# Optimization experiments

Hardware: AMD Instinct MI355X
Metric: run time of the kernel (lower is better)

Reference implementation:

```python
import jax, jax.numpy as jnp
import numpy as np

EMBED = 1024
HEADS = 16
HEAD_DIM = EMBED // HEADS
FF = 4 * EMBED
B, S = 2, 2048


def setup_inputs() -> dict:
    key = jax.random.key(0)
    ks = jax.random.split(key, 16)
    sd = 0.02
    inp = {
        "x": jax.random.normal(ks[0], (B, S, EMBED), dtype=jnp.float32),
        "Wq": jax.random.normal(ks[1], (EMBED, EMBED), dtype=jnp.float32) * sd,
        "bq": jnp.zeros((EMBED,), jnp.float32),
        "Wk": jax.random.normal(ks[2], (EMBED, EMBED), dtype=jnp.float32) * sd,
        "bk": jnp.zeros((EMBED,), jnp.float32),
        "Wv": jax.random.normal(ks[3], (EMBED, EMBED), dtype=jnp.float32) * sd,
        "bv": jnp.zeros((EMBED,), jnp.float32),
        "Wo": jax.random.normal(ks[4], (EMBED, EMBED), dtype=jnp.float32) * sd,
        "W1": jax.random.normal(ks[5], (EMBED, FF), dtype=jnp.float32) * sd,
        "b1": jnp.zeros((FF,), jnp.float32),
        "W2": jax.random.normal(ks[6], (FF, EMBED), dtype=jnp.float32) * sd,
        "b2": jnp.zeros((EMBED,), jnp.float32),
        "g1": jnp.ones((EMBED,), jnp.float32),
        "be1": jnp.zeros((EMBED,), jnp.float32),
        "g2": jnp.ones((EMBED,), jnp.float32),
        "be2": jnp.zeros((EMBED,), jnp.float32),
    }
    return inp


def _layernorm(x, g, b, eps=1e-5):
    mu = jnp.mean(x, axis=-1, keepdims=True)
    var = jnp.mean(jnp.square(x - mu), axis=-1, keepdims=True)
    return (x - mu) * jax.lax.rsqrt(var + eps) * g + b


def _attn(x, Wq, bq, Wk, bk, Wv, bv, Wo):
    b, s, d = x.shape
    q = (x @ Wq + bq).reshape(b, s, HEADS, HEAD_DIM)
    k = (x @ Wk + bk).reshape(b, s, HEADS, HEAD_DIM)
    v = (x @ Wv + bv).reshape(b, s, HEADS, HEAD_DIM)
    # NOTE: original scales by sqrt(embed_dim), NOT sqrt(head_dim)
    logits = jnp.einsum('bqhd,bkhd->bhqk', q, k) / jnp.sqrt(jnp.float32(d))
    mask = jnp.tril(jnp.ones((s, s), dtype=bool))
    logits = jnp.where(mask, logits, -jnp.inf)
    w = jax.nn.softmax(logits, axis=-1)
    z = jnp.einsum('bhqk,bkhd->bqhd', w, v).reshape(b, s, d)
    return z @ Wo


def reference(x, Wq, bq, Wk, bk, Wv, bv, Wo, W1, b1, W2, b2, g1, be1, g2, be2):
    h = x + _attn(_layernorm(x, g1, be1), Wq, bq, Wk, bk, Wv, bv, Wo)
    m = _layernorm(h, g2, be2)
    m = jax.nn.gelu(m @ W1 + b1, approximate=False) @ W2 + b2
    return h + m
```

## Files before the change

kernel.cpp:

```cpp
#include <hip/hip_runtime.h>
#include <cstdint>
#include <cstddef>
#include <math.h>

#define EMBED 1024
#define SEQ   2048
#define NROWS 4096
#define NHEADS 16

typedef __bf16 bf16x8 __attribute__((ext_vector_type(8)));
typedef float f32x4 __attribute__((ext_vector_type(4)));
typedef unsigned short us8 __attribute__((ext_vector_type(8)));
typedef unsigned short us4 __attribute__((ext_vector_type(4)));

__device__ __forceinline__ unsigned short f2bf(float f) {
  union { float f; unsigned u; } v; v.f = f;
  unsigned r = v.u + 0x7fffu + ((v.u >> 16) & 1u);
  return (unsigned short)(r >> 16);
}

__device__ __forceinline__ bf16x8 as_bf(us8 u) { return __builtin_bit_cast(bf16x8, u); }

__device__ __forceinline__ void gload_lds16(const unsigned short* g, unsigned short* l) {
  __builtin_amdgcn_global_load_lds((const __attribute__((address_space(1))) void*)g,
                                   (__attribute__((address_space(3))) void*)l, 16, 0, 0);
}

__global__ __launch_bounds__(256) void transpose_to_bf16(
    const float* __restrict__ in, unsigned short* __restrict__ out, int K, int N) {
  __shared__ float tile[32][33];
  const int tx = threadIdx.x & 31, ty = threadIdx.x >> 5;
  const int n0 = blockIdx.x * 32, k0 = blockIdx.y * 32;
#pragma unroll
  for (int i = 0; i < 4; i++) {
    int k = ty + i * 8;
    tile[k][tx] = in[(size_t)(k0 + k) * N + n0 + tx];
  }
  __syncthreads();
#pragma unroll
  for (int i = 0; i < 4; i++) {
    int n = ty + i * 8;
    out[(size_t)(n0 + n) * K + k0 + tx] = f2bf(tile[tx][n]);
  }
}

__global__ __launch_bounds__(256) void layernorm_bf16(
    const float* __restrict__ x, const float* __restrict__ g,
    const float* __restrict__ be, unsigned short* __restrict__ out) {
  const int wave = threadIdx.x >> 6, lane = threadIdx.x & 63;
  const int row = blockIdx.x * 4 + wave;
  const float* xr = x + (size_t)row * EMBED;
  float4 v[4];
  float s = 0.f, sq = 0.f;
#pragma unroll
  for (int c = 0; c < 4; c++) {
    v[c] = *(const float4*)&xr[c * 256 + lane * 4];
    s  += v[c].x + v[c].y + v[c].z + v[c].w;
    sq += v[c].x * v[c].x + v[c].y * v[c].y + v[c].z * v[c].z + v[c].w * v[c].w;
  }
#pragma unroll
  for (int m = 1; m < 64; m <<= 1) {
    s  += __shfl_xor(s, m, 64);
    sq += __shfl_xor(sq, m, 64);
  }
  const float mean = s * (1.f / 1024.f);
  const float var  = sq * (1.f / 1024.f) - mean * mean;
  const float rstd = rsqrtf(var + 1e-5f);
#pragma unroll
  for (int c = 0; c < 4; c++) {
    const int idx = c * 256 + lane * 4;
    us4 o;
    o[0] = f2bf((v[c].x - mean) * rstd * g[idx + 0] + be[idx + 0]);
    o[1] = f2bf((v[c].y - mean) * rstd * g[idx + 1] + be[idx + 1]);
    o[2] = f2bf((v[c].z - mean) * rstd * g[idx + 2] + be[idx + 2]);
    o[3] = f2bf((v[c].w - mean) * rstd * g[idx + 3] + be[idx + 3]);
    *(us4*)&out[(size_t)row * EMBED + idx] = o;
  }
}

enum { MODE_QKV = 0, MODE_WO = 1, MODE_FF1 = 2, MODE_FF2 = 3 };

template <int MODE>
__global__ __launch_bounds__(256) void gemm_bf16(
    const unsigned short* __restrict__ A,
    const unsigned short* __restrict__ Bt0,
    const unsigned short* __restrict__ Bt1,
    const unsigned short* __restrict__ Bt2,
    const float* __restrict__ bias0,
    const float* __restrict__ bias1,
    const float* __restrict__ bias2,
    const float* __restrict__ res,
    void* __restrict__ out0, void* __restrict__ out1, void* __restrict__ out2,
    int M, int N, int K) {
  const unsigned short* Bt = Bt0;
  const float* bias = bias0;
  void* outv = out0;
  int zidx = 0;
  if constexpr (MODE == MODE_QKV) {
    zidx = blockIdx.z;
    if (zidx == 1)      { Bt = Bt1; bias = bias1; outv = out1; }
    else if (zidx == 2) { Bt = Bt2; bias = bias2; outv = out2; }
  }
  __shared__ unsigned short As[128 * 32];
  __shared__ unsigned short Bs[128 * 32];
  const int tid = threadIdx.x;
  const int wave = tid >> 6, lane = tid & 63;
  const int quad = lane >> 4, l15 = lane & 15;
  const int wr = (wave >> 1) * 64, wc = (wave & 1) * 64;
  const int rowA0 = blockIdx.y * 128, colB0 = blockIdx.x * 128;

  const int srow = tid >> 2;
  const int scol = (tid & 3) * 8;
  const unsigned short* gA = A  + (size_t)(rowA0 + srow) * K + scol;
  const unsigned short* gB = Bt + (size_t)(colB0 + srow) * K + scol;
  unsigned short* lA  = &As[tid * 8];
  unsigned short* lA2 = &As[2048 + tid * 8];
  unsigned short* lB  = &Bs[tid * 8];
  unsigned short* lB2 = &Bs[2048 + tid * 8];
  const size_t half = (size_t)64 * K;

  f32x4 acc[4][4];
#pragma unroll
  for (int i = 0; i < 4; i++)
#pragma unroll
    for (int j = 0; j < 4; j++) acc[i][j] = f32x4{0.f, 0.f, 0.f, 0.f};

  for (int k0 = 0; k0 < K; k0 += 32) {
    gload_lds16(gA + k0, lA);
    gload_lds16(gA + half + k0, lA2);
    gload_lds16(gB + k0, lB);
    gload_lds16(gB + half + k0, lB2);
    __syncthreads();
    bf16x8 af[4], bfr[4];
#pragma unroll
    for (int mi = 0; mi < 4; mi++)
      af[mi] = as_bf(*(const us8*)&As[(wr + mi * 16 + l15) * 32 + quad * 8]);
#pragma unroll
    for (int ni = 0; ni < 4; ni++)
      bfr[ni] = as_bf(*(const us8*)&Bs[(wc + ni * 16 + l15) * 32 + quad * 8]);
#pragma unroll
    for (int mi = 0; mi < 4; mi++)
#pragma unroll
      for (int ni = 0; ni < 4; ni++)
        acc[mi][ni] = __builtin_amdgcn_mfma_f32_16x16x32_bf16(af[mi], bfr[ni], acc[mi][ni], 0, 0, 0);
    __syncthreads();
  }

#pragma unroll
  for (int ni = 0; ni < 4; ni++) {
    const int col = colB0 + wc + ni * 16 + l15;
    float bv = 0.f;
    if constexpr (MODE != MODE_WO) bv = bias[col];
#pragma unroll
    for (int mi = 0; mi < 4; mi++) {
      const int row0 = rowA0 + wr + mi * 16 + quad * 4;
      if constexpr (MODE == MODE_QKV) {
        unsigned short* o = (unsigned short*)outv;
        if (zidx == 2) {
          us4 pk;
#pragma unroll
          for (int r = 0; r < 4; r++) pk[r] = f2bf(acc[mi][ni][r] + bv);
          const int bb = row0 >> 11;
          const int sr = row0 & 2047;
          *(us4*)&o[((size_t)(bb * 1024 + col)) * SEQ + sr] = pk;
        } else {
#pragma unroll
          for (int r = 0; r < 4; r++)
            o[(size_t)(row0 + r) * N + col] = f2bf(acc[mi][ni][r] + bv);
        }
      } else if constexpr (MODE == MODE_FF1) {
        unsigned short* o = (unsigned short*)outv;
#pragma unroll
        for (int r = 0; r < 4; r++) {
          float v = acc[mi][ni][r] + bv;
          v = 0.5f * v * (1.f + erff(v * 0.7071067811865476f));
          o[(size_t)(row0 + r) * N + col] = f2bf(v);
        }
      } else {
        float* o = (float*)outv;
#pragma unroll
        for (int r = 0; r < 4; r++) {
          float v = acc[mi][ni][r] + bv + res[(size_t)(row0 + r) * N + col];
          o[(size_t)(row0 + r) * N + col] = v;
        }
      }
    }
  }
}

__global__ __launch_bounds__(256) void attn_kernel(
    const unsigned short* __restrict__ Q,
    const unsigned short* __restrict__ Kb,
    const unsigned short* __restrict__ Vt,
    unsigned short* __restrict__ Z) {
  __shared__ unsigned short Ksh[2][64][32];
  __shared__ unsigned short Vsh[2][64][32];
  __shared__ unsigned short Pt[4][16][72];
  __shared__ float Ot[4][64][17];

  const int wave = threadIdx.x >> 6, lane = threadIdx.x & 63;
  const int quad = lane >> 4, l15 = lane & 15;
  const int bh = blockIdx.x, b = bh >> 4, h = bh & 15;
  const int qt = blockIdx.y;
  const int q0 = qt * 128 + wave * 32;
  const float cscale = 1.4426950408889634f / 32.f;

  bf16x8 qf[2][2];
#pragma unroll
  for (int c = 0; c < 2; c++)
#pragma unroll
    for (int kf = 0; kf < 2; kf++)
      qf[c][kf] = as_bf(*(const us8*)&Q[(size_t)(b * SEQ + q0 + c * 16 + l15) * EMBED +
                                        h * 64 + kf * 32 + quad * 8]);

  f32x4 accO[2][4];
#pragma unroll
  for (int c = 0; c < 2; c++)
#pragma unroll
    for (int dt = 0; dt < 4; dt++) accO[c][dt] = f32x4{0.f, 0.f, 0.f, 0.f};
  float mrun[2] = {-INFINITY, -INFINITY};
  float lrun[2] = {0.f, 0.f};

  const int ls_row = lane >> 2;
  const int ls_c16 = lane & 3;
  const int nkt = 2 * qt + 2;

  for (int kt = 0; kt < nkt; kt++) {
    const int kbase = kt * 64;
    const int krow = wave * 16 + ls_row;
#pragma unroll
    for (int kf = 0; kf < 2; kf++) {
      const unsigned short* g =
          &Kb[(size_t)(b * SEQ + kbase + krow) * EMBED + h * 64 + kf * 32 + ls_c16 * 8];
      gload_lds16(g, &Ksh[kf][wave * 16][0] + lane * 8);
    }
#pragma unroll
    for (int kk = 0; kk < 2; kk++) {
      const unsigned short* g =
          &Vt[(size_t)(b * 1024 + h * 64 + krow) * SEQ + kbase + kk * 32 + ls_c16 * 8];
      gload_lds16(g, &Vsh[kk][wave * 16][0] + lane * 8);
    }
    __syncthreads();

#pragma unroll
    for (int c = 0; c < 2; c++) {
      const int qc = q0 + c * 16;
      if (kbase > qc + 15) continue;
      f32x4 sf[4];
#pragma unroll
      for (int nt = 0; nt < 4; nt++) {
        f32x4 z4 = f32x4{0.f, 0.f, 0.f, 0.f};
#pragma unroll
        for (int kf = 0; kf < 2; kf++) {
          const bf16x8 ka = as_bf(*(const us8*)&Ksh[kf][nt * 16 + l15][quad * 8]);
          z4 = __builtin_amdgcn_mfma_f32_16x16x32_bf16(ka, qf[c][kf], z4, 0, 0, 0);
        }
        sf[nt] = z4 * cscale;
      }
      if (kbase + 63 > qc) {
        const int q = qc + l15;
#pragma unroll
        for (int nt = 0; nt < 4; nt++) {
          const int key0 = kbase + nt * 16 + quad * 4;
#pragma unroll
          for (int r = 0; r < 4; r++)
            if (key0 + r > q) sf[nt][r] = -INFINITY;
        }
      }
      float mx = sf[0][0];
#pragma unroll
      for (int nt = 0; nt < 4; nt++)
#pragma unroll
        for (int r = 0; r < 4; r++) mx = fmaxf(mx, sf[nt][r]);
      mx = fmaxf(mx, __shfl_xor(mx, 16, 64));
      mx = fmaxf(mx, __shfl_xor(mx, 32, 64));
      const float mnew = fmaxf(mrun[c], mx);
      const float alpha = exp2f(mrun[c] - mnew);
      mrun[c] = mnew;
      float rs = 0.f;
#pragma unroll
      for (int nt = 0; nt < 4; nt++) {
        us4 pk;
#pragma unroll
        for (int r = 0; r < 4; r++) {
          const float p = exp2f(sf[nt][r] - mnew);
          rs += p;
          pk[r] = f2bf(p);
        }
        *(us4*)&Pt[wave][l15][nt * 16 + quad * 4] = pk;
      }
      rs += __shfl_xor(rs, 16, 64);
      rs += __shfl_xor(rs, 32, 64);
      lrun[c] = lrun[c] * alpha + rs;
#pragma unroll
      for (int dt = 0; dt < 4; dt++) accO[c][dt] = accO[c][dt] * alpha;
      bf16x8 pf[2];
#pragma unroll
      for (int kk = 0; kk < 2; kk++)
        pf[kk] = as_bf(*(const us8*)&Pt[wave][l15][kk * 32 + quad * 8]);
#pragma unroll
      for (int dt = 0; dt < 4; dt++)
#pragma unroll
        for (int kk = 0; kk < 2; kk++) {
          const bf16x8 va = as_bf(*(const us8*)&Vsh[kk][dt * 16 + l15][quad * 8]);
          accO[c][dt] = __builtin_amdgcn_mfma_f32_16x16x32_bf16(va, pf[kk], accO[c][dt], 0, 0, 0);
        }
    }
    __syncthreads();
  }

#pragma unroll
  for (int c = 0; c < 2; c++) {
    const float inv = 1.f / lrun[c];
#pragma unroll
    for (int dt = 0; dt < 4; dt++)
#pragma unroll
      for (int r = 0; r < 4; r++)
        Ot[wave][dt * 16 + quad * 4 + r][l15] = accO[c][dt][r] * inv;
    const int lq = lane >> 2, dbase = (lane & 3) * 16;
    us8 o0, o1;
#pragma unroll
    for (int i = 0; i < 8; i++) o0[i] = f2bf(Ot[wave][dbase + i][lq]);
#pragma unroll
    for (int i = 0; i < 8; i++) o1[i] = f2bf(Ot[wave][dbase + 8 + i][lq]);
    unsigned short* zp = Z + (size_t)(b * SEQ + q0 + c * 16 + lq) * EMBED + h * 64 + dbase;
    *(us8*)zp = o0;
    *(us8*)(zp + 8) = o1;
  }
}

extern "C" void kernel_launch(void* const* d_in, const int* in_sizes, int n_in,
                              void* d_out, int out_size, void* d_ws, size_t ws_size,
                              hipStream_t stream) {
  const float* x   = (const float*)d_in[0];
  const float* Wq  = (const float*)d_in[1];
  const float* bq  = (const float*)d_in[2];
  const float* Wk  = (const float*)d_in[3];
  const float* bk  = (const float*)d_in[4];
  const float* Wv  = (const float*)d_in[5];
  const float* bv  = (const float*)d_in[6];
  const float* Wo  = (const float*)d_in[7];
  const float* W1  = (const float*)d_in[8];
  const float* b1  = (const float*)d_in[9];
  const float* W2  = (const float*)d_in[10];
  const float* b2  = (const float*)d_in[11];
  const float* g1  = (const float*)d_in[12];
  const float* be1 = (const float*)d_in[13];
  const float* g2  = (const float*)d_in[14];
  const float* be2 = (const float*)d_in[15];
  float* out = (float*)d_out;

  char* ws = (char*)d_ws;
  const size_t MB = 1024 * 1024;
  unsigned short* wqT = (unsigned short*)(ws + 0 * MB);
  unsigned short* wkT = (unsigned short*)(ws + 2 * MB);
  unsigned short* wvT = (unsigned short*)(ws + 4 * MB);
  unsigned short* woT = (unsigned short*)(ws + 6 * MB);
  unsigned short* w1T = (unsigned short*)(ws + 8 * MB);
  unsigned short* w2T = (unsigned short*)(ws + 16 * MB);
  float*          hb  = (float*)         (ws + 24 * MB);
  unsigned short* ln1 = (unsigned short*)(ws + 40 * MB);
  unsigned short* qb  = (unsigned short*)(ws + 48 * MB);
  unsigned short* kb2 = (unsigned short*)(ws + 56 * MB);
  unsigned short* vT  = (unsigned short*)(ws + 64 * MB);
  unsigned short* zb  = (unsigned short*)(ws + 72 * MB);
  unsigned short* ln2 = (unsigned short*)(ws + 80 * MB);
  unsigned short* m1  = (unsigned short*)(ws + 40 * MB);
  (void)in_sizes; (void)n_in; (void)out_size; (void)ws_size;

  transpose_to_bf16<<<dim3(32, 32), 256, 0, stream>>>(Wq, wqT, 1024, 1024);
  transpose_to_bf16<<<dim3(32, 32), 256, 0, stream>>>(Wk, wkT, 1024, 1024);
  transpose_to_bf16<<<dim3(32, 32), 256, 0, stream>>>(Wv, wvT, 1024, 1024);
  transpose_to_bf16<<<dim3(32, 32), 256, 0, stream>>>(Wo, woT, 1024, 1024);
  transpose_to_bf16<<<dim3(128, 32), 256, 0, stream>>>(W1, w1T, 1024, 4096);
  transpose_to_bf16<<<dim3(32, 128), 256, 0, stream>>>(W2, w2T, 4096, 1024);

  layernorm_bf16<<<NROWS / 4, 256, 0, stream>>>(x, g1, be1, ln1);

  gemm_bf16<MODE_QKV><<<dim3(8, 32, 3), 256, 0, stream>>>(
      ln1, wqT, wkT, wvT, bq, bk, bv, nullptr, qb, kb2, vT, NROWS, 1024, 1024);

  attn_kernel<<<dim3(32, 16), 256, 0, stream>>>(qb, kb2, vT, zb);

  gemm_bf16<MODE_WO><<<dim3(8, 32), 256, 0, stream>>>(
      zb, woT, nullptr, nullptr, nullptr, nullptr, nullptr, x, hb, nullptr, nullptr,
      NROWS, 1024, 1024);

  layernorm_bf16<<<NROWS / 4, 256, 0, stream>>>(hb, g2, be2, ln2);

  gemm_bf16<MODE_FF1><<<dim3(32, 32), 256, 0, stream>>>(
      ln2, w1T, nullptr, nullptr, b1, nullptr, nullptr, nullptr, m1, nullptr, nullptr,
      NROWS, 4096, 1024);

  gemm_bf16<MODE_FF2><<<dim3(8, 32), 256, 0, stream>>>(
      m1, w2T, nullptr, nullptr, b2, nullptr, nullptr, hb, out, nullptr, nullptr,
      NROWS, 1024, 4096);
}
```

Before: 460.3 us.

## Split-K the FF2 GEMM four ways with bf16 partials and a reduce kernel

The FF2 GEMM (K=4096) is split into four K-slices launched along grid z, so it runs 1024 blocks instead of 256 and fills the GPU better. Each slice writes a bf16 partial tile. A new elementwise kernel then sums the four partials with the residual and bias into the fp32 output. To fit the partials, workspace buffers are reassigned to reuse regions that are dead by that point. The cost is extra partial-buffer traffic, one more launch, and lower precision from rounding the partial sums to bf16.

```diff
diff --git a/kernel.cpp b/kernel.cpp
--- a/kernel.cpp
+++ b/kernel.cpp
@@ -17,6 +17,9 @@
   union { float f; unsigned u; } v; v.f = f;
   unsigned r = v.u + 0x7fffu + ((v.u >> 16) & 1u);
   return (unsigned short)(r >> 16);
+}
+__device__ __forceinline__ float bf2f(unsigned short u) {
+  union { unsigned u; float f; } v; v.u = (unsigned)u << 16; return v.f;
 }
 
 __device__ __forceinline__ bf16x8 as_bf(us8 u) { return __builtin_bit_cast(bf16x8, u); }
@@ -78,7 +81,7 @@
   }
 }
 
-enum { MODE_QKV = 0, MODE_WO = 1, MODE_FF1 = 2, MODE_FF2 = 3 };
+enum { MODE_QKV = 0, MODE_WO = 1, MODE_FF1 = 2, MODE_FF2 = 3, MODE_PART = 4 };
 
 template <int MODE>
 __global__ __launch_bounds__(256) void gemm_bf16(
@@ -90,7 +93,8 @@
     const float* __restrict__ bias1,
     const float* __restrict__ bias2,
     const float* __restrict__ res,
-    void* __restrict__ out0, void* __restrict__ out1, void* __restrict__ out2,
+    void* __restrict__ out0, void* __restrict__ out1,
+    void* __restrict__ out2, void* __restrict__ out3,
     int M, int N, int K) {
   const unsigned short* Bt = Bt0;
   const float* bias = bias0;
@@ -101,6 +105,13 @@
     if (zidx == 1)      { Bt = Bt1; bias = bias1; outv = out1; }
     else if (zidx == 2) { Bt = Bt2; bias = bias2; outv = out2; }
   }
+  if constexpr (MODE == MODE_PART) {
+    zidx = blockIdx.z;
+    outv = (zidx == 0) ? out0 : (zidx == 1) ? out1 : (zidx == 2) ? out2 : out3;
+  }
+  const int Ksub = (MODE == MODE_PART) ? 1024 : K;
+  const int koff = (MODE == MODE_PART) ? zidx * 1024 : 0;
+
   __shared__ unsigned short As[128 * 32];
   __shared__ unsigned short Bs[128 * 32];
   const int tid = threadIdx.x;
@@ -111,8 +122,8 @@
 
   const int srow = tid >> 2;
   const int scol = (tid & 3) * 8;
-  const unsigned short* gA = A  + (size_t)(rowA0 + srow) * K + scol;
-  const unsigned short* gB = Bt + (size_t)(colB0 + srow) * K + scol;
+  const unsigned short* gA = A  + (size_t)(rowA0 + srow) * K + koff + scol;
+  const unsigned short* gB = Bt + (size_t)(colB0 + srow) * K + koff + scol;
   unsigned short* lA  = &As[tid * 8];
   unsigned short* lA2 = &As[2048 + tid * 8];
   unsigned short* lB  = &Bs[tid * 8];
@@ -125,7 +136,7 @@
 #pragma unroll
     for (int j = 0; j < 4; j++) acc[i][j] = f32x4{0.f, 0.f, 0.f, 0.f};
 
-  for (int k0 = 0; k0 < K; k0 += 32) {
+  for (int k0 = 0; k0 < Ksub; k0 += 32) {
     gload_lds16(gA + k0, lA);
     gload_lds16(gA + half + k0, lA2);
     gload_lds16(gB + k0, lB);
@@ -150,7 +161,7 @@
   for (int ni = 0; ni < 4; ni++) {
     const int col = colB0 + wc + ni * 16 + l15;
     float bv = 0.f;
-    if constexpr (MODE != MODE_WO) bv = bias[col];
+    if constexpr (MODE == MODE_QKV || MODE == MODE_FF1 || MODE == MODE_FF2) bv = bias[col];
 #pragma unroll
     for (int mi = 0; mi < 4; mi++) {
       const int row0 = rowA0 + wr + mi * 16 + quad * 4;
@@ -176,6 +187,11 @@
           v = 0.5f * v * (1.f + erff(v * 0.7071067811865476f));
           o[(size_t)(row0 + r) * N + col] = f2bf(v);
         }
+      } else if constexpr (MODE == MODE_PART) {
+        unsigned short* o = (unsigned short*)outv;
+#pragma unroll
+        for (int r = 0; r < 4; r++)
+          o[(size_t)(row0 + r) * N + col] = f2bf(acc[mi][ni][r]);
       } else {
         float* o = (float*)outv;
 #pragma unroll
@@ -186,6 +202,27 @@
       }
     }
   }
+}
+
+__global__ __launch_bounds__(256) void ff2_reduce(
+    const float* __restrict__ hb, const float* __restrict__ b2,
+    const unsigned short* __restrict__ p0, const unsigned short* __restrict__ p1,
+    const unsigned short* __restrict__ p2, const unsigned short* __restrict__ p3,
+    float* __restrict__ out) {
+  const size_t i = ((size_t)blockIdx.x * 256 + threadIdx.x) * 4;
+  const int col = (int)(i & (EMBED - 1));
+  const float4 h = *(const float4*)&hb[i];
+  const float4 bb = *(const float4*)&b2[col];
+  const us4 a = *(const us4*)&p0[i];
+  const us4 b = *(const us4*)&p1[i];
+  const us4 c = *(const us4*)&p2[i];
+  const us4 d = *(const us4*)&p3[i];
+  float4 o;
+  o.x = h.x + bb.x + bf2f(a[0]) + bf2f(b[0]) + bf2f(c[0]) + bf2f(d[0]);
+  o.y = h.y + bb.y + bf2f(a[1]) + bf2f(b[1]) + bf2f(c[1]) + bf2f(d[1]);
+  o.z = h.z + bb.z + bf2f(a[2]) + bf2f(b[2]) + bf2f(c[2]) + bf2f(d[2]);
+  o.w = h.w + bb.w + bf2f(a[3]) + bf2f(b[3]) + bf2f(c[3]) + bf2f(d[3]);
+  *(float4*)&out[i] = o;
 }
 
 __global__ __launch_bounds__(256) void attn_kernel(
@@ -358,14 +395,18 @@
   unsigned short* woT = (unsigned short*)(ws + 6 * MB);
   unsigned short* w1T = (unsigned short*)(ws + 8 * MB);
   unsigned short* w2T = (unsigned short*)(ws + 16 * MB);
-  float*          hb  = (float*)         (ws + 24 * MB);
-  unsigned short* ln1 = (unsigned short*)(ws + 40 * MB);
-  unsigned short* qb  = (unsigned short*)(ws + 48 * MB);
-  unsigned short* kb2 = (unsigned short*)(ws + 56 * MB);
-  unsigned short* vT  = (unsigned short*)(ws + 64 * MB);
-  unsigned short* zb  = (unsigned short*)(ws + 72 * MB);
-  unsigned short* ln2 = (unsigned short*)(ws + 80 * MB);
-  unsigned short* m1  = (unsigned short*)(ws + 40 * MB);
+  unsigned short* ln1 = (unsigned short*)(ws + 24 * MB);
+  unsigned short* qb  = (unsigned short*)(ws + 32 * MB);
+  unsigned short* kb2 = (unsigned short*)(ws + 40 * MB);
+  unsigned short* vT  = (unsigned short*)(ws + 48 * MB);
+  unsigned short* zb  = (unsigned short*)(ws + 24 * MB);
+  float*          hb  = (float*)         (ws + 32 * MB);
+  unsigned short* ln2 = (unsigned short*)(ws + 48 * MB);
+  unsigned short* m1  = (unsigned short*)(ws + 56 * MB);
+  unsigned short* p0  = (unsigned short*)(ws + 0 * MB);
+  unsigned short* p1  = (unsigned short*)(ws + 8 * MB);
+  unsigned short* p2  = (unsigned short*)(ws + 24 * MB);
+  unsigned short* p3  = (unsigned short*)(ws + 48 * MB);
   (void)in_sizes; (void)n_in; (void)out_size; (void)ws_size;
 
   transpose_to_bf16<<<dim3(32, 32), 256, 0, stream>>>(Wq, wqT, 1024, 1024);
@@ -378,21 +419,25 @@
   layernorm_bf16<<<NROWS / 4, 256, 0, stream>>>(x, g1, be1, ln1);
 
   gemm_bf16<MODE_QKV><<<dim3(8, 32, 3), 256, 0, stream>>>(
-      ln1, wqT, wkT, wvT, bq, bk, bv, nullptr, qb, kb2, vT, NROWS, 1024, 1024);
+      ln1, wqT, wkT, wvT, bq, bk, bv, nullptr, qb, kb2, vT, nullptr,
+      NROWS, 1024, 1024);
 
   attn_kernel<<<dim3(32, 16), 256, 0, stream>>>(qb, kb2, vT, zb);
 
   gemm_bf16<MODE_WO><<<dim3(8, 32), 256, 0, stream>>>(
-      zb, woT, nullptr, nullptr, nullptr, nullptr, nullptr, x, hb, nullptr, nullptr,
-      NROWS, 1024, 1024);
+      zb, woT, nullptr, nullptr, nullptr, nullptr, nullptr, x,
+      hb, nullptr, nullptr, nullptr, NROWS, 1024, 1024);
 
   layernorm_bf16<<<NROWS / 4, 256, 0, stream>>>(hb, g2, be2, ln2);
 
   gemm_bf16<MODE_FF1><<<dim3(32, 32), 256, 0, stream>>>(
-      ln2, w1T, nullptr, nullptr, b1, nullptr, nullptr, nullptr, m1, nullptr, nullptr,
-      NROWS, 4096, 1024);
-
-  gemm_bf16<MODE_FF2><<<dim3(8, 32), 256, 0, stream>>>(
-      m1, w2T, nullptr, nullptr, b2, nullptr, nullptr, hb, out, nullptr, nullptr,
-      NROWS, 1024, 4096);
-}
+      ln2, w1T, nullptr, nullptr, b1, nullptr, nullptr, nullptr,
+      m1, nullptr, nullptr, nullptr, NROWS, 4096, 1024);
+
+  gemm_bf16<MODE_PART><<<dim3(8, 32, 4), 256, 0, stream>>>(
+      m1, w2T, nullptr, nullptr, nullptr, nullptr, nullptr, nullptr,
+      p0, p1, p2, p3, NROWS, 1024, 4096);
+
+  ff2_reduce<<<NROWS * EMBED / (256 * 4), 256, 0, stream>>>(
+      hb, b2, p0, p1, p2, p3, out);
+}
```

Measured after the change: 439.0 us. 4.6% less time.
